# Optimization experiments

Hardware: AMD Instinct MI355X
Metric: run time of the kernel (lower is better)

The kernel has to match this reference:

```python
import jax, jax.numpy as jnp
import numpy as np

LAYERS = 2      # LightGCN propagation layers
LAMB = 0.5      # aux loss weight
REG = 1e-4      # embedding reg weight
N_AUX = 2       # len(behaviors) - 1


def setup_inputs() -> dict:
    key = jax.random.key(0)
    k = jax.random.split(key, 8)
    n_users, n_items, d = 100000, 50000, 32
    E = 1000000
    user_emb = (jax.random.normal(k[0], (n_users + 1, d), jnp.float32) * 0.1).at[0].set(0.0)
    item_emb = (jax.random.normal(k[1], (n_items + 1, d), jnp.float32) * 0.1).at[0].set(0.0)
    aux_u = jax.random.randint(k[2], (N_AUX, E), 1, n_users + 1)
    aux_i = jax.random.randint(k[3], (N_AUX, E), 1, n_items + 1)
    aux_edges = jnp.stack([aux_u, aux_i], axis=-1).astype(jnp.int32)
    tgt_u = jax.random.randint(k[4], (E,), 1, n_users + 1)
    tgt_i = jax.random.randint(k[5], (E,), 1, n_items + 1)
    target_edges = jnp.stack([tgt_u, tgt_i], axis=-1).astype(jnp.int32)
    # [B, 1+N_AUX, 3]: per row (user, pos_item, neg_item) for target then each aux behavior
    batch_data = jax.random.randint(k[6], (4096, 1 + N_AUX, 3), 1, n_items + 1).astype(jnp.int32)
    return {"user_emb": user_emb, "item_emb": item_emb, "batch_data": batch_data,
            "aux_edges": aux_edges, "target_edges": target_edges}


def _graph(edges, n_user_rows, N):
    """Symmetric-normalized bipartite LightGCN graph as directed COO (src, dst, w)."""
    u = edges[:, 0]
    v = edges[:, 1] + n_user_rows  # shift item ids into joint node space
    ones = jnp.ones(u.shape[0], jnp.float32)
    deg = jax.ops.segment_sum(ones, u, num_segments=N) + jax.ops.segment_sum(ones, v, num_segments=N)
    dinv = jnp.where(deg > 0, jax.lax.rsqrt(jnp.maximum(deg, 1.0)), 0.0)
    w = dinv[u] * dinv[v]
    src = jnp.concatenate([u, v])
    dst = jnp.concatenate([v, u])
    w2 = jnp.concatenate([w, w])
    return src, dst, w2


def _lightgcn(emb, src, dst, w, N):
    """L-layer LightGCN propagation, mean over layers 0..L."""
    acc = emb
    cur = emb
    for _ in range(LAYERS):
        cur = jax.ops.segment_sum(w[:, None] * cur[src], dst, num_segments=N)
        acc = acc + cur
    return acc / (LAYERS + 1)


def _prob(ue, ie, u, i):
    return jax.nn.relu(jnp.sum(ue[u] * ie[i], axis=-1))


def _bpr(p, n):
    return -jnp.mean(jax.nn.log_sigmoid(p - n))


def reference(user_emb, item_emb, batch_data, aux_edges, target_edges):
    Nu = user_emb.shape[0]
    N = Nu + item_emb.shape[0]
    all_emb = jnp.concatenate([user_emb, item_emb], axis=0)
    tgt_g = _graph(target_edges, Nu, N)

    user, p_item, n_item = batch_data[:, 0, 0], batch_data[:, 0, 1], batch_data[:, 0, 2]
    aux_user, aux_p, aux_n = batch_data[:, 1:, 0], batch_data[:, 1:, 1], batch_data[:, 1:, 2]

    cps, cns, dps, dns, aps, ans, aux_losses = [], [], [], [], [], [], []
    for idx in range(N_AUX):
        # combine graph = aux behavior edges union target edges
        comb_edges = jnp.concatenate([aux_edges[idx], target_edges], axis=0)
        ce = _lightgcn(all_emb, *_graph(comb_edges, Nu, N), N)
        cu, ci = ce[:Nu], ce[Nu:]
        cps.append(_prob(cu, ci, user, p_item))
        cns.append(_prob(cu, ci, user, n_item))

        ae = _lightgcn(all_emb, *_graph(aux_edges[idx], Nu, N), N)
        au, ai = ae[:Nu], ae[Nu:]
        aps.append(_prob(au, ai, user, p_item))
        ans.append(_prob(au, ai, user, n_item))

        # condition: propagate aux embeddings through the target graph
        de = _lightgcn(ae, *tgt_g, N)
        du, di = de[:Nu], de[Nu:]
        dps.append(_prob(du, di, user, p_item))
        dns.append(_prob(du, di, user, n_item))

        ps = jnp.sum(au[aux_user[:, idx]] * ai[aux_p[:, idx]], axis=-1)
        ns = jnp.sum(au[aux_user[:, idx]] * ai[aux_n[:, idx]], axis=-1)
        aux_losses.append(_bpr(ps, ns))

    aux_loss = jnp.mean(jnp.stack(aux_losses))

    def front_door(cond, comb, aux):
        return jnp.sum(cond * jnp.sum(comb * aux, axis=0), axis=0)

    p_scores = front_door(jnp.stack(dps), jnp.stack(cps), jnp.stack(aps))
    n_scores = front_door(jnp.stack(dns), jnp.stack(cns), jnp.stack(ans))
    rec_loss = _bpr(p_scores, n_scores)
    emb_loss = (jnp.linalg.norm(user_emb) + jnp.linalg.norm(item_emb)) / item_emb.shape[0]
    return rec_loss + LAMB * aux_loss + REG * emb_loss
```

## Files before the change

kernel.cpp:

```cpp
#include <hip/hip_runtime.h>
#include <hip/hip_fp16.h>
#include <math.h>

#define D 32
#define ROWU 16
#define NBK 1024
#define BSHIFT 8
#define TILE_H 16384
#define TILE_BIN 2048

typedef unsigned int u32;
typedef unsigned short u16;

__device__ __forceinline__ float logsigf(float x) {
  return fminf(x, 0.f) - log1pf(expf(-fabsf(x)));
}

__device__ __forceinline__ float lo16(u32 u) { return __uint_as_float(u << 16); }
__device__ __forceinline__ float hi16(u32 u) { return __uint_as_float(u & 0xFFFF0000u); }
__device__ __forceinline__ u32 pk2(float a, float b) {
  u32 ua = __float_as_uint(a), ub = __float_as_uint(b);
  u32 ra = (ua + 0x7FFFu + ((ua >> 16) & 1u)) >> 16;
  u32 rb = (ub + 0x7FFFu + ((ub >> 16) & 1u)) >> 16;
  return (ra & 0xFFFFu) | (rb << 16);
}
__device__ __forceinline__ float bfat(const u16* __restrict__ p, size_t off) {
  return __uint_as_float(((u32)p[off]) << 16);
}
__device__ __forceinline__ void accum8(float* a, float w, uint4 x) {
  a[0] += w * lo16(x.x); a[1] += w * hi16(x.x);
  a[2] += w * lo16(x.y); a[3] += w * hi16(x.y);
  a[4] += w * lo16(x.z); a[5] += w * hi16(x.z);
  a[6] += w * lo16(x.w); a[7] += w * hi16(x.w);
}
__device__ __forceinline__ uint4 pack8(const float* a, float w) {
  return make_uint4(pk2(w * a[0], w * a[1]), pk2(w * a[2], w * a[3]),
                    pk2(w * a[4], w * a[5]), pk2(w * a[6], w * a[7]));
}

__device__ __forceinline__ int wpack(float a, float b) {
  __half2 h = __floats2half2_rn(a, b);
  return *reinterpret_cast<int*>(&h);
}
__device__ __forceinline__ float2 hun(int wb) {
  __half2 h;
  *reinterpret_cast<int*>(&h) = wb;
  return __half22float2(h);
}


__global__ void hist_kernel(const int2* __restrict__ tgt, const int2* __restrict__ aux,
                            int E, int Nu, int BPS, int* __restrict__ bcur) {
  __shared__ int lh[NBK];
  int seg = blockIdx.x / BPS;
  int blk = blockIdx.x - seg * BPS;
  const int2* edges = (seg == 0) ? tgt : aux + (size_t)(seg - 1) * E;
  for (int b = threadIdx.x; b < NBK; b += 256) lh[b] = 0;
  __syncthreads();
  int e0 = blk * TILE_H;
  for (int k = threadIdx.x; k < TILE_H; k += 256) {
    int e = e0 + k;
    if (e < E) {
      int2 ed = edges[e];
      atomicAdd(&lh[ed.x >> BSHIFT], 1);
      atomicAdd(&lh[(ed.y + Nu) >> BSHIFT], 1);
    }
  }
  __syncthreads();
  for (int b = threadIdx.x; b < NBK; b += 256)
    if (lh[b]) atomicAdd(&bcur[seg * NBK + b], lh[b]);
}

__global__ void bscan_kernel(int* __restrict__ bcur) {
  int* b = bcur + blockIdx.x * NBK;
  int lane = threadIdx.x;
  int carry = 0;
  for (int base = 0; base < NBK; base += 64) {
    int i = base + lane;
    int v = b[i];
    int s = v;
    #pragma unroll
    for (int o = 1; o < 64; o <<= 1) {
      int t = __shfl_up(s, o);
      if (lane >= o) s += t;
    }
    b[i] = carry + s - v;
    carry += __shfl(s, 63);
  }
}

__global__ void bin_kernel(const int2* __restrict__ tgt, const int2* __restrict__ aux,
                           int E, int Nu, int BPS, int* __restrict__ bcur,
                           int* __restrict__ binned) {
  __shared__ int stage[2 * TILE_BIN];
  __shared__ int lh[NBK];
  __shared__ int loff[NBK];
  __shared__ int gb[NBK];
  __shared__ int wred[4];
  __shared__ int stot;
  int seg = blockIdx.x / BPS;
  int blk = blockIdx.x - seg * BPS;
  const int2* edges = (seg == 0) ? tgt : aux + (size_t)(seg - 1) * E;
  int* out = binned + (size_t)seg * 2 * E;
  int tid = threadIdx.x;
  for (int b = tid; b < NBK; b += 256) lh[b] = 0;
  __syncthreads();
  int e0 = blk * TILE_BIN;
  int pkv[16];
  int pb[16];
  int pr[16];
  #pragma unroll
  for (int it = 0; it < 8; ++it) {
    int e = e0 + tid + it * 256;
    bool ok = e < E;
    int2 ed = ok ? edges[e] : make_int2(0, -Nu);
    int u = ed.x, v = ed.y + Nu;
    int b1 = u >> BSHIFT, b2 = v >> BSHIFT;
    pkv[2 * it] = ((u & 255) << 18) | v;
    pb[2 * it] = b1;
    pr[2 * it] = ok ? atomicAdd(&lh[b1], 1) : 0;
    pkv[2 * it + 1] = ((v & 255) << 18) | u;
    pb[2 * it + 1] = b2;
    pr[2 * it + 1] = ok ? atomicAdd(&lh[b2], 1) : 0;
  }
  __syncthreads();
  int lane = tid & 63, wid = tid >> 6;
  int b4 = tid * 4;
  int v0 = lh[b4], v1 = lh[b4 + 1], v2 = lh[b4 + 2], v3 = lh[b4 + 3];
  int tsum = v0 + v1 + v2 + v3;
  int incl = tsum;
  #pragma unroll
  for (int o = 1; o < 64; o <<= 1) {
    int t = __shfl_up(incl, o);
    if (lane >= o) incl += t;
  }
  if (lane == 63) wred[wid] = incl;
  __syncthreads();
  int wbase = 0;
  for (int w = 0; w < wid; ++w) wbase += wred[w];
  int excl = wbase + incl - tsum;
  loff[b4] = excl;
  loff[b4 + 1] = excl + v0;
  loff[b4 + 2] = excl + v0 + v1;
  loff[b4 + 3] = excl + v0 + v1 + v2;
  if (tid == 255) stot = excl + tsum;
  #pragma unroll
  for (int j = 0; j < 4; ++j) {
    int b = b4 + j;
    int c = lh[b];
    gb[b] = c ? atomicAdd(&bcur[seg * NBK + b], c) : 0;
  }
  __syncthreads();
  #pragma unroll
  for (int it = 0; it < 16; ++it) {
    int e = e0 + tid + (it >> 1) * 256;
    if (e < E) stage[loff[pb[it]] + pr[it]] = pkv[it];
  }
  __syncthreads();
  int tot = stot;
  for (int k = tid; k < tot; k += 256) {
    int lo = 0, hi = NBK;
    while (lo < hi) {
      int mid = (lo + hi) >> 1;
      if (loff[mid] <= k) lo = mid + 1; else hi = mid;
    }
    int b = lo - 1;
    out[gb[b] + (k - loff[b])] = stage[k];
  }
}

__global__ void csr_count_kernel(const int* __restrict__ binned,
                                 const int* __restrict__ bend, int E2, int N, int NBKe,
                                 int* __restrict__ deg3, int* __restrict__ rp3) {
  __shared__ int cnt[256];
  __shared__ int wred[4];
  int seg = blockIdx.x / NBKe;
  int bkt = blockIdx.x - seg * NBKe;
  int node0 = bkt << BSHIFT;
  const int* bc = bend + seg * NBK;
  int start = (bkt == 0) ? 0 : bc[bkt - 1];
  int end = bc[bkt];
  int cntE = end - start;
  const int* src = binned + (size_t)seg * E2 + start;
  cnt[threadIdx.x] = 0;
  __syncthreads();
  for (int k = threadIdx.x; k < cntE; k += 256) atomicAdd(&cnt[src[k] >> 18], 1);
  __syncthreads();
  int lane = threadIdx.x & 63, wid = threadIdx.x >> 6;
  int v = cnt[threadIdx.x];
  int incl = v;
  #pragma unroll
  for (int o = 1; o < 64; o <<= 1) {
    int t = __shfl_up(incl, o);
    if (lane >= o) incl += t;
  }
  if (lane == 63) wred[wid] = incl;
  __syncthreads();
  int wbase = 0;
  for (int w = 0; w < wid; ++w) wbase += wred[w];
  int node = node0 + (int)threadIdx.x;
  if (node < N) {
    deg3[(size_t)seg * N + node] = v;
    rp3[(size_t)seg * (N + 1) + node] = start + wbase + incl - v;
  }
  if (bkt == 0 && threadIdx.x == 0) rp3[(size_t)seg * (N + 1) + N] = E2;
}

__global__ void dinv_all_kernel(const int* __restrict__ deg3, float* __restrict__ dinv5,
                                int N) {
  int n = blockIdx.x * blockDim.x + threadIdx.x;
  if (n >= N) return;
  int dt = deg3[n], d0 = deg3[N + n], d1 = deg3[2 * N + n];
  dinv5[n]         = dt ? rsqrtf((float)dt) : 0.f;
  dinv5[N + n]     = d0 ? rsqrtf((float)d0) : 0.f;
  dinv5[2 * N + n] = d1 ? rsqrtf((float)d1) : 0.f;
  int c0 = dt + d0, c1 = dt + d1;
  dinv5[3 * N + n] = c0 ? rsqrtf((float)c0) : 0.f;
  dinv5[4 * N + n] = c1 ? rsqrtf((float)c1) : 0.f;
}

__global__ void csr_scatter_kernel(const int* __restrict__ binned,
                                   const int* __restrict__ bend,
                                   const int* __restrict__ rp3,
                                   const float* __restrict__ dinv5,
                                   int E2, int N, int NBKe,
                                   int2* __restrict__ pk) {
  __shared__ int cnt[256];
  __shared__ int off[256];
  int seg = blockIdx.x / NBKe;
  int bkt = blockIdx.x - seg * NBKe;
  int node0 = bkt << BSHIFT;
  const int* bc = bend + seg * NBK;
  int start = (bkt == 0) ? 0 : bc[bkt - 1];
  int end = bc[bkt];
  int cntE = end - start;
  const int* src = binned + (size_t)seg * E2 + start;
  int node = node0 + (int)threadIdx.x;
  off[threadIdx.x] = (node < N) ? rp3[(size_t)seg * (N + 1) + node] : 0;
  cnt[threadIdx.x] = 0;
  const float* dvL = dinv5 + (size_t)(seg == 0 ? 3 : seg) * N;
  const float* dvH = dinv5 + (size_t)(seg == 0 ? 4 : seg + 2) * N;
  __syncthreads();
  int2* out = pk + (size_t)seg * E2;
  for (int k = threadIdx.x; k < cntE; k += 256) {
    int en = src[k];
    int lb = en >> 18;
    int c = en & 0x3FFFF;
    int pos = atomicAdd(&cnt[lb], 1);
    out[off[lb] + pos] = make_int2(c, wpack(dvL[c], dvH[c]));
  }
}

__global__ void cvt_emb_kernel(const float2* __restrict__ ue, long nu2,
                               const float2* __restrict__ ie, long ni2,
                               u32* __restrict__ emb) {
  long i = (long)blockIdx.x * blockDim.x + threadIdx.x;
  if (i >= nu2 + ni2) return;
  float2 v = (i < nu2) ? ue[i] : ie[i - nu2];
  emb[i] = pk2(v.x, v.y);
}


__global__ void gather_fused_all_kernel(const int* __restrict__ rp3,
                                        const int2* __restrict__ pk,
                                        const float* __restrict__ dinv5,
                                        const uint4* __restrict__ emb,
                                        uint4* __restrict__ BaAll, uint4* __restrict__ BcAll,
                                        int N, int E2) {
  const int* rpA0 = rp3 + (size_t)(N + 1);
  const int* rpA1 = rp3 + 2 * (size_t)(N + 1);
  const int2* pT = pk;
  const int2* pA0 = pk + (size_t)E2;
  const int2* pA1 = pk + 2 * (size_t)E2;
  const float* dvA0 = dinv5 + (size_t)N;
  const float* dvA1 = dinv5 + 2 * (size_t)N;
  const float* dvC0 = dinv5 + 3 * (size_t)N;
  const float* dvC1 = dinv5 + 4 * (size_t)N;
  int t = blockIdx.x * blockDim.x + threadIdx.x;
  int n = t >> 2;
  if (n >= N) return;
  int lane = t & 3;
  int qb = (threadIdx.x & 63) & 60;
  float aA0[8] = {0, 0, 0, 0, 0, 0, 0, 0};
  float aA1[8] = {0, 0, 0, 0, 0, 0, 0, 0};
  float aC0[8] = {0, 0, 0, 0, 0, 0, 0, 0};
  float aC1[8] = {0, 0, 0, 0, 0, 0, 0, 0};
  int s = rpA0[n], e = rpA0[n + 1];
  int j = s;
  for (; j + 3 < e; j += 4) {
    int2 en = pA0[j + lane];
    #pragma unroll
    for (int q = 0; q < 4; ++q) {
      int c = __shfl(en.x, qb + q);
      float2 w = hun(__shfl(en.y, qb + q));
      uint4 x = emb[(size_t)c * 4 + lane];
      accum8(aA0, w.x, x);
      accum8(aC0, w.y, x);
    }
  }
  for (; j < e; ++j) {
    int2 en = pA0[j];
    float2 w = hun(en.y);
    uint4 x = emb[(size_t)en.x * 4 + lane];
    accum8(aA0, w.x, x);
    accum8(aC0, w.y, x);
  }
  s = rpA1[n]; e = rpA1[n + 1];
  j = s;
  for (; j + 3 < e; j += 4) {
    int2 en = pA1[j + lane];
    #pragma unroll
    for (int q = 0; q < 4; ++q) {
      int c = __shfl(en.x, qb + q);
      float2 w = hun(__shfl(en.y, qb + q));
      uint4 x = emb[(size_t)c * 4 + lane];
      accum8(aA1, w.x, x);
      accum8(aC1, w.y, x);
    }
  }
  for (; j < e; ++j) {
    int2 en = pA1[j];
    float2 w = hun(en.y);
    uint4 x = emb[(size_t)en.x * 4 + lane];
    accum8(aA1, w.x, x);
    accum8(aC1, w.y, x);
  }
  s = rp3[n]; e = rp3[n + 1];
  j = s;
  for (; j + 3 < e; j += 4) {
    int2 en = pT[j + lane];
    #pragma unroll
    for (int q = 0; q < 4; ++q) {
      int c = __shfl(en.x, qb + q);
      float2 w = hun(__shfl(en.y, qb + q));
      uint4 x = emb[(size_t)c * 4 + lane];
      accum8(aC0, w.x, x);
      accum8(aC1, w.y, x);
    }
  }
  for (; j < e; ++j) {
    int2 en = pT[j];
    float2 w = hun(en.y);
    uint4 x = emb[(size_t)en.x * 4 + lane];
    accum8(aC0, w.x, x);
    accum8(aC1, w.y, x);
  }
  size_t o = (size_t)n * 4 + lane;
  size_t rowN4 = (size_t)N * 4;
  BaAll[o] = pack8(aA0, dvA0[n]);
  BaAll[rowN4 + o] = pack8(aA1, dvA1[n]);
  BcAll[o] = pack8(aC0, dvC0[n]);
  BcAll[rowN4 + o] = pack8(aC1, dvC1[n]);
}

__global__ void gather_avg_kernel(const int* __restrict__ rp3, const int2* __restrict__ pk,
                                  const float* __restrict__ dinv5,
                                  const uint4* __restrict__ emb,
                                  const uint4* __restrict__ BaAll, uint4* __restrict__ AI,
                                  int N, int E2) {
  int idx = blockIdx.y;
  const int* rp = rp3 + (size_t)(1 + idx) * (N + 1);
  const int2* pA = pk + (size_t)(1 + idx) * E2;
  const float* dv = dinv5 + (size_t)(1 + idx) * N;
  const uint4* cur = BaAll + (size_t)idx * N * 4;
  int t = blockIdx.x * blockDim.x + threadIdx.x;
  int n = t >> 2;
  if (n >= N) return;
  int lane = t & 3;
  int qb = (threadIdx.x & 63) & 60;
  float acc[8] = {0, 0, 0, 0, 0, 0, 0, 0};
  int s = rp[n], e = rp[n + 1];
  int j = s;
  for (; j + 3 < e; j += 4) {
    int2 en = pA[j + lane];
    #pragma unroll
    for (int q = 0; q < 4; ++q) {
      int c = __shfl(en.x, qb + q);
      float2 w = hun(__shfl(en.y, qb + q));
      uint4 x = cur[(size_t)c * 4 + lane];
      accum8(acc, w.x, x);
    }
  }
  for (; j < e; ++j) {
    int2 en = pA[j];
    float2 w = hun(en.y);
    uint4 x = cur[(size_t)en.x * 4 + lane];
    accum8(acc, w.x, x);
  }
  float wn = dv[n];
  uint4 e4 = emb[(size_t)n * 4 + lane];
  uint4 b4 = cur[(size_t)n * 4 + lane];
  float r[8];
  r[0] = (lo16(e4.x) + lo16(b4.x) + wn * acc[0]) * (1.f / 3.f);
  r[1] = (hi16(e4.x) + hi16(b4.x) + wn * acc[1]) * (1.f / 3.f);
  r[2] = (lo16(e4.y) + lo16(b4.y) + wn * acc[2]) * (1.f / 3.f);
  r[3] = (hi16(e4.y) + hi16(b4.y) + wn * acc[3]) * (1.f / 3.f);
  r[4] = (lo16(e4.z) + lo16(b4.z) + wn * acc[4]) * (1.f / 3.f);
  r[5] = (hi16(e4.z) + hi16(b4.z) + wn * acc[5]) * (1.f / 3.f);
  r[6] = (lo16(e4.w) + lo16(b4.w) + wn * acc[6]) * (1.f / 3.f);
  r[7] = (hi16(e4.w) + hi16(b4.w) + wn * acc[7]) * (1.f / 3.f);
  AI[(size_t)n * 8 + idx * 4 + lane] = pack8(r, 1.f);
}

__global__ void de_gather_kernel(const int* __restrict__ rp3, const int2* __restrict__ pk,
                                 const float* __restrict__ dinv5,
                                 const uint4* __restrict__ AI, uint4* __restrict__ DeI,
                                 int N) {
  int t = blockIdx.x * blockDim.x + threadIdx.x;
  int n = t >> 3;
  if (n >= N) return;
  int lane = t & 7;
  int gb = (threadIdx.x & 63) & 56;
  float acc[8] = {0, 0, 0, 0, 0, 0, 0, 0};
  int s = rp3[n], e = rp3[n + 1];
  int j = s;
  for (; j + 3 < e; j += 4) {
    int2 en = pk[j + (lane & 3)];
    #pragma unroll
    for (int q = 0; q < 4; ++q) {
      int c = __shfl(en.x, gb + q);
      float w = dinv5[c];
      uint4 x = AI[(size_t)c * 8 + lane];
      accum8(acc, w, x);
    }
  }
  for (; j < e; ++j) {
    int2 en = pk[j];
    float w = dinv5[en.x];
    uint4 x = AI[(size_t)en.x * 8 + lane];
    accum8(acc, w, x);
  }
  DeI[(size_t)n * 8 + lane] = pack8(acc, dinv5[n]);
}


__device__ __forceinline__ float fdim2(const int2* __restrict__ pkA, const int2* __restrict__ pkT,
                                       const int* __restrict__ rpA, const int* __restrict__ rpT,
                                       int idx, const float* __restrict__ dv,
                                       const u16* __restrict__ base, const u16* __restrict__ L1,
                                       int r, int d) {
  float acc = 0.f;
  for (int j = rpA[r]; j < rpA[r + 1]; ++j) {
    int2 en = pkA[j];
    acc += hun(en.y).y * bfat(L1, (size_t)en.x * D + d);
  }
  for (int j = rpT[r]; j < rpT[r + 1]; ++j) {
    int2 en = pkT[j];
    float2 w = hun(en.y);
    acc += (idx ? w.y : w.x) * bfat(L1, (size_t)en.x * D + d);
  }
  return (bfat(base, (size_t)r * D + d) + bfat(L1, (size_t)r * D + d) + dv[r] * acc) * (1.f / 3.f);
}

__device__ __forceinline__ float fdim1i(const int2* __restrict__ pkT, const int* __restrict__ rp,
                                        const float* __restrict__ dv,
                                        const u16* __restrict__ base, const u16* __restrict__ L1,
                                        int r, int di) {
  float acc = 0.f;
  for (int j = rp[r]; j < rp[r + 1]; ++j) {
    int2 en = pkT[j];
    acc += dv[en.x] * bfat(L1, (size_t)en.x * 64 + di);
  }
  return (bfat(base, (size_t)r * 64 + di) + bfat(L1, (size_t)r * 64 + di) + dv[r] * acc) * (1.f / 3.f);
}

__global__ void ce_sparse_kernel(const int* __restrict__ rp3, const int2* __restrict__ pk,
                                 const float* __restrict__ dinv5,
                                 const u32* __restrict__ EMBu, const u32* __restrict__ BcAll,
                                 const int* __restrict__ batch, int Bsz, int Nu, int N, int E2,
                                 float* __restrict__ cps, float* __restrict__ cns) {
  int idx = blockIdx.y;
  const int* rpA = rp3 + (size_t)(1 + idx) * (N + 1);
  const int2* pkA = pk + (size_t)(1 + idx) * E2;
  const float* dv = dinv5 + (size_t)(3 + idx) * N;
  const u16* base = (const u16*)EMBu;
  const u16* L1 = (const u16*)(BcAll + (size_t)idx * N * ROWU);
  float* outp = cps + (size_t)idx * Bsz;
  float* outn = cns + (size_t)idx * Bsz;
  int t = blockIdx.x * blockDim.x + threadIdx.x;
  int b = t >> 5, d = t & 31;
  if (b >= Bsz) return;
  int u = batch[b * 9 + 0];
  int p = batch[b * 9 + 1] + Nu;
  int n = batch[b * 9 + 2] + Nu;
  float uv = fdim2(pkA, pk, rpA, rp3, idx, dv, base, L1, u, d);
  float pv = fdim2(pkA, pk, rpA, rp3, idx, dv, base, L1, p, d);
  float nv = fdim2(pkA, pk, rpA, rp3, idx, dv, base, L1, n, d);
  float sp = uv * pv, sn = uv * nv;
  #pragma unroll
  for (int o = 16; o > 0; o >>= 1) {
    sp += __shfl_down(sp, o, 32);
    sn += __shfl_down(sn, o, 32);
  }
  if (d == 0) {
    outp[b] = fmaxf(sp, 0.f);
    outn[b] = fmaxf(sn, 0.f);
  }
}

__global__ void de_sparse_kernel(const int* __restrict__ rp3, const int2* __restrict__ pk,
                                 const float* __restrict__ dinv5,
                                 const u32* __restrict__ AI, const u32* __restrict__ DeI,
                                 const int* __restrict__ batch, int Bsz, int Nu, int N,
                                 float* __restrict__ dps, float* __restrict__ dns) {
  int idx = blockIdx.y;
  const u16* base = (const u16*)AI;
  const u16* L1 = (const u16*)DeI;
  float* outp = dps + (size_t)idx * Bsz;
  float* outn = dns + (size_t)idx * Bsz;
  int t = blockIdx.x * blockDim.x + threadIdx.x;
  int b = t >> 5, d = t & 31;
  if (b >= Bsz) return;
  int di = idx * 32 + d;
  int u = batch[b * 9 + 0];
  int p = batch[b * 9 + 1] + Nu;
  int n = batch[b * 9 + 2] + Nu;
  float uv = fdim1i(pk, rp3, dinv5, base, L1, u, di);
  float pv = fdim1i(pk, rp3, dinv5, base, L1, p, di);
  float nv = fdim1i(pk, rp3, dinv5, base, L1, n, di);
  float sp = uv * pv, sn = uv * nv;
  #pragma unroll
  for (int o = 16; o > 0; o >>= 1) {
    sp += __shfl_down(sp, o, 32);
    sn += __shfl_down(sn, o, 32);
  }
  if (d == 0) {
    outp[b] = fmaxf(sp, 0.f);
    outn[b] = fmaxf(sn, 0.f);
  }
}


__device__ __forceinline__ float dotrow(const u32* __restrict__ a, const u32* __restrict__ b) {
  float s = 0.f;
  #pragma unroll
  for (int k = 0; k < ROWU; ++k) {
    u32 x = a[k], y = b[k];
    s += lo16(x) * lo16(y) + hi16(x) * hi16(y);
  }
  return s;
}

__global__ void score_aux_kernel(const u32* __restrict__ AI, const int* __restrict__ batch,
                                 int Bsz, int Nu, int N, float* __restrict__ aps,
                                 float* __restrict__ ans_, float* __restrict__ accs) {
  int idx = blockIdx.y;
  const u32* A = AI + (size_t)idx * ROWU;
  float* outp = aps + (size_t)idx * Bsz;
  float* outn = ans_ + (size_t)idx * Bsz;
  int b = blockIdx.x * blockDim.x + threadIdx.x;
  float l = 0.f;
  if (b < Bsz) {
    int u = batch[b * 9 + 0];
    int p = batch[b * 9 + 1] + Nu;
    int n = batch[b * 9 + 2] + Nu;
    const u32* ur = A + (size_t)u * 32;
    outp[b] = fmaxf(dotrow(ur, A + (size_t)p * 32), 0.f);
    outn[b] = fmaxf(dotrow(ur, A + (size_t)n * 32), 0.f);
    const int* r = batch + b * 9 + 3 * (1 + idx);
    const u32* aur = A + (size_t)r[0] * 32;
    float ps = dotrow(aur, A + (size_t)(r[1] + Nu) * 32);
    float ns = dotrow(aur, A + (size_t)(r[2] + Nu) * 32);
    l = -logsigf(ps - ns);
  }
  for (int o = 32; o > 0; o >>= 1) l += __shfl_down(l, o);
  if ((threadIdx.x & 63) == 0) atomicAdd(&accs[idx], l);
}

__global__ void recloss_kernel(const float* __restrict__ cps, const float* __restrict__ cns,
                               const float* __restrict__ aps, const float* __restrict__ ans_,
                               const float* __restrict__ dps, const float* __restrict__ dns,
                               int Bsz, int NA, float* __restrict__ acc) {
  int b = blockIdx.x * blockDim.x + threadIdx.x;
  float l = 0.f;
  if (b < Bsz) {
    float dp = 0.f, dn = 0.f, cap = 0.f, can = 0.f;
    for (int i = 0; i < NA; ++i) {
      dp += dps[i * Bsz + b];
      dn += dns[i * Bsz + b];
      cap += cps[i * Bsz + b] * aps[i * Bsz + b];
      can += cns[i * Bsz + b] * ans_[i * Bsz + b];
    }
    l = -logsigf(dp * cap - dn * can);
  }
  for (int o = 32; o > 0; o >>= 1) l += __shfl_down(l, o);
  if ((threadIdx.x & 63) == 0) atomicAdd(acc, l);
}

__global__ void sumsq2_kernel(const float4* __restrict__ xu, int n4u,
                              const float4* __restrict__ xi, int n4i,
                              float* __restrict__ accU, float* __restrict__ accI) {
  __shared__ float redU[4], redI[4];
  int tid = threadIdx.x;
  int gid = blockIdx.x * blockDim.x + tid;
  int stride = gridDim.x * blockDim.x;
  float su = 0.f, si = 0.f;
  for (int i = gid; i < n4u; i += stride) {
    float4 v = xu[i];
    su += v.x * v.x + v.y * v.y + v.z * v.z + v.w * v.w;
  }
  for (int i = gid; i < n4i; i += stride) {
    float4 v = xi[i];
    si += v.x * v.x + v.y * v.y + v.z * v.z + v.w * v.w;
  }
  for (int o = 32; o > 0; o >>= 1) {
    su += __shfl_down(su, o);
    si += __shfl_down(si, o);
  }
  if ((tid & 63) == 0) { redU[tid >> 6] = su; redI[tid >> 6] = si; }
  __syncthreads();
  if (tid == 0) {
    atomicAdd(accU, redU[0] + redU[1] + redU[2] + redU[3]);
    atomicAdd(accI, redI[0] + redI[1] + redI[2] + redI[3]);
  }
}

__global__ void final_kernel(const float* __restrict__ accs, int Bsz, int NA, int NiRows,
                             float* __restrict__ out) {
  float rec = accs[NA] / (float)Bsz;
  float aux = 0.f;
  for (int i = 0; i < NA; ++i) aux += accs[i] / (float)Bsz;
  aux /= (float)NA;
  float embl = (sqrtf(accs[NA + 1]) + sqrtf(accs[NA + 2])) / (float)NiRows;
  out[0] = rec + 0.5f * aux + 1e-4f * embl;
}

extern "C" void kernel_launch(void* const* d_in, const int* in_sizes, int n_in,
                              void* d_out, int out_size, void* d_ws, size_t ws_size,
                              hipStream_t stream) {
  const float* user_emb = (const float*)d_in[0];
  const float* item_emb = (const float*)d_in[1];
  const int* batch = (const int*)d_in[2];
  const int* aux_edges = (const int*)d_in[3];
  const int* tgt_edges = (const int*)d_in[4];

  const int NuRows = in_sizes[0] / D;
  const int NiRows = in_sizes[1] / D;
  const int Bsz = in_sizes[2] / 9;
  const int E = in_sizes[4] / 2;
  const int NA = in_sizes[3] / (2 * E);
  const int N = NuRows + NiRows;
  const int E2 = 2 * E;
  const size_t rowH = (size_t)N * ROWU;
  const int BPS_H = (E + TILE_H - 1) / TILE_H;
  const int BPS_B = (E + TILE_BIN - 1) / TILE_BIN;
  const int NBKe = (N + (1 << BSHIFT) - 1) >> BSHIFT;

  u32* EMBu = (u32*)d_ws;
  u32* AI = EMBu + rowH;
  u32* BaAll = AI + 2 * rowH;
  u32* BcAll = BaAll + 2 * rowH;
  int* deg3 = (int*)(BcAll + 2 * rowH);
  float* dinv5 = (float*)(deg3 + 3 * (size_t)N);
  int* rp3 = (int*)(dinv5 + 5 * (size_t)N);
  int* bcur = rp3 + 3 * (size_t)(N + 1);
  uintptr_t pka = ((uintptr_t)(bcur + 3 * (size_t)NBK) + 7) & ~(uintptr_t)7;
  int2* pk = (int2*)pka;
  float* cps = (float*)(pk + 3 * (size_t)E2);
  float* cns = cps + (size_t)NA * Bsz;
  float* aps = cns + (size_t)NA * Bsz;
  float* ans_ = aps + (size_t)NA * Bsz;
  float* dps = ans_ + (size_t)NA * Bsz;
  float* dns = dps + (size_t)NA * Bsz;
  float* accs = dns + (size_t)NA * Bsz;
  int* binned = (int*)AI;

  const int TB = 256;
  const int gN = (N + TB - 1) / TB;
  const int gN4 = (N * 4 + TB - 1) / TB;
  const int gN8 = (N * 8 + TB - 1) / TB;
  const int gB = (Bsz + TB - 1) / TB;
  const int gB32 = (Bsz * 32 + TB - 1) / TB;
  const long nu2 = (long)NuRows * ROWU;
  const long ni2 = (long)NiRows * ROWU;
  const int gCvt = (int)((nu2 + ni2 + TB - 1) / TB);

  cvt_emb_kernel<<<gCvt, TB, 0, stream>>>((const float2*)user_emb, nu2,
                                          (const float2*)item_emb, ni2, EMBu);

  hipMemsetAsync(bcur, 0, 3 * (size_t)NBK * sizeof(int), stream);
  hist_kernel<<<3 * BPS_H, TB, 0, stream>>>((const int2*)tgt_edges, (const int2*)aux_edges,
                                            E, NuRows, BPS_H, bcur);
  bscan_kernel<<<3, 64, 0, stream>>>(bcur);
  bin_kernel<<<3 * BPS_B, TB, 0, stream>>>((const int2*)tgt_edges, (const int2*)aux_edges,
                                           E, NuRows, BPS_B, bcur, binned);
  csr_count_kernel<<<3 * NBKe, TB, 0, stream>>>(binned, bcur, E2, N, NBKe, deg3, rp3);
  dinv_all_kernel<<<gN, TB, 0, stream>>>(deg3, dinv5, N);
  csr_scatter_kernel<<<3 * NBKe, TB, 0, stream>>>(binned, bcur, rp3, dinv5, E2, N, NBKe, pk);

  hipMemsetAsync(accs, 0, (size_t)(NA + 3) * sizeof(float), stream);

  dim3 gridG(gN4, NA), gridB(gB, NA), gridS(gB32, NA);

  gather_fused_all_kernel<<<gN4, TB, 0, stream>>>(rp3, pk, dinv5, (const uint4*)EMBu,
                                                  (uint4*)BaAll, (uint4*)BcAll, N, E2);
  gather_avg_kernel<<<gridG, TB, 0, stream>>>(rp3, pk, dinv5, (const uint4*)EMBu,
                                              (const uint4*)BaAll, (uint4*)AI, N, E2);
  score_aux_kernel<<<gridB, TB, 0, stream>>>(AI, batch, Bsz, NuRows, N, aps, ans_, accs);
  ce_sparse_kernel<<<gridS, TB, 0, stream>>>(rp3, pk, dinv5, EMBu, BcAll,
                                             batch, Bsz, NuRows, N, E2, cps, cns);
  de_gather_kernel<<<gN8, TB, 0, stream>>>(rp3, pk, dinv5, (const uint4*)AI,
                                           (uint4*)BaAll, N);
  de_sparse_kernel<<<gridS, TB, 0, stream>>>(rp3, pk, dinv5, AI, (const u32*)BaAll,
                                             batch, Bsz, NuRows, N, dps, dns);

  sumsq2_kernel<<<104, TB, 0, stream>>>((const float4*)user_emb,
                                        (int)((size_t)NuRows * D / 4),
                                        (const float4*)item_emb,
                                        (int)((size_t)NiRows * D / 4),
                                        accs + NA + 1, accs + NA + 2);
  recloss_kernel<<<gB, TB, 0, stream>>>(cps, cns, aps, ans_, dps, dns, Bsz, NA, accs + NA);
  final_kernel<<<1, 1, 0, stream>>>(accs, Bsz, NA, NiRows, (float*)d_out);
}
```

Before: 668.0 us.

## Vectorize CSR edge loads, store bucket ids in bin stage, precompute weight table

```diff
diff --git a/kernel.cpp b/kernel.cpp
--- a/kernel.cpp
+++ b/kernel.cpp
@@ -38,9 +38,9 @@
                     pk2(w * a[4], w * a[5]), pk2(w * a[6], w * a[7]));
 }
 
-__device__ __forceinline__ int wpack(float a, float b) {
+__device__ __forceinline__ u32 wpack(float a, float b) {
   __half2 h = __floats2half2_rn(a, b);
-  return *reinterpret_cast<int*>(&h);
+  return *reinterpret_cast<u32*>(&h);
 }
 __device__ __forceinline__ float2 hun(int wb) {
   __half2 h;
@@ -93,6 +93,7 @@
                            int E, int Nu, int BPS, int* __restrict__ bcur,
                            int* __restrict__ binned) {
   __shared__ int stage[2 * TILE_BIN];
+  __shared__ u16 stagebk[2 * TILE_BIN];
   __shared__ int lh[NBK];
   __shared__ int loff[NBK];
   __shared__ int gb[NBK];
@@ -154,17 +155,16 @@
   #pragma unroll
   for (int it = 0; it < 16; ++it) {
     int e = e0 + tid + (it >> 1) * 256;
-    if (e < E) stage[loff[pb[it]] + pr[it]] = pkv[it];
+    if (e < E) {
+      int pos = loff[pb[it]] + pr[it];
+      stage[pos] = pkv[it];
+      stagebk[pos] = (u16)pb[it];
+    }
   }
   __syncthreads();
   int tot = stot;
   for (int k = tid; k < tot; k += 256) {
-    int lo = 0, hi = NBK;
-    while (lo < hi) {
-      int mid = (lo + hi) >> 1;
-      if (loff[mid] <= k) lo = mid + 1; else hi = mid;
-    }
-    int b = lo - 1;
+    int b = stagebk[k];
     out[gb[b] + (k - loff[b])] = stage[k];
   }
 }
@@ -207,22 +207,30 @@
 }
 
 __global__ void dinv_all_kernel(const int* __restrict__ deg3, float* __restrict__ dinv5,
-                                int N) {
+                                u32* __restrict__ wtab, int N) {
   int n = blockIdx.x * blockDim.x + threadIdx.x;
   if (n >= N) return;
   int dt = deg3[n], d0 = deg3[N + n], d1 = deg3[2 * N + n];
-  dinv5[n]         = dt ? rsqrtf((float)dt) : 0.f;
-  dinv5[N + n]     = d0 ? rsqrtf((float)d0) : 0.f;
-  dinv5[2 * N + n] = d1 ? rsqrtf((float)d1) : 0.f;
+  float wt  = dt ? rsqrtf((float)dt) : 0.f;
+  float wa0 = d0 ? rsqrtf((float)d0) : 0.f;
+  float wa1 = d1 ? rsqrtf((float)d1) : 0.f;
   int c0 = dt + d0, c1 = dt + d1;
-  dinv5[3 * N + n] = c0 ? rsqrtf((float)c0) : 0.f;
-  dinv5[4 * N + n] = c1 ? rsqrtf((float)c1) : 0.f;
+  float wc0 = c0 ? rsqrtf((float)c0) : 0.f;
+  float wc1 = c1 ? rsqrtf((float)c1) : 0.f;
+  dinv5[n] = wt;
+  dinv5[N + n] = wa0;
+  dinv5[2 * N + n] = wa1;
+  dinv5[3 * N + n] = wc0;
+  dinv5[4 * N + n] = wc1;
+  wtab[n] = wpack(wc0, wc1);
+  wtab[N + n] = wpack(wa0, wc0);
+  wtab[2 * N + n] = wpack(wa1, wc1);
 }
 
 __global__ void csr_scatter_kernel(const int* __restrict__ binned,
                                    const int* __restrict__ bend,
                                    const int* __restrict__ rp3,
-                                   const float* __restrict__ dinv5,
+                                   const u32* __restrict__ wtab,
                                    int E2, int N, int NBKe,
                                    int2* __restrict__ pk) {
   __shared__ int cnt[256];
@@ -238,8 +246,7 @@
   int node = node0 + (int)threadIdx.x;
   off[threadIdx.x] = (node < N) ? rp3[(size_t)seg * (N + 1) + node] : 0;
   cnt[threadIdx.x] = 0;
-  const float* dvL = dinv5 + (size_t)(seg == 0 ? 3 : seg) * N;
-  const float* dvH = dinv5 + (size_t)(seg == 0 ? 4 : seg + 2) * N;
+  const u32* wt = wtab + (size_t)seg * N;
   __syncthreads();
   int2* out = pk + (size_t)seg * E2;
   for (int k = threadIdx.x; k < cntE; k += 256) {
@@ -247,7 +254,7 @@
     int lb = en >> 18;
     int c = en & 0x3FFFF;
     int pos = atomicAdd(&cnt[lb], 1);
-    out[off[lb] + pos] = make_int2(c, wpack(dvL[c], dvH[c]));
+    out[off[lb] + pos] = make_int2(c, (int)wt[c]);
   }
 }
 
@@ -260,6 +267,38 @@
   emb[i] = pk2(v.x, v.y);
 }
 
+
+__device__ __forceinline__ void edge1_dual(const int2* __restrict__ p, int j, int lane,
+                                           const uint4* __restrict__ rows,
+                                           float* a1, float* a2) {
+  int2 en = p[j];
+  float2 w = hun(en.y);
+  uint4 x = rows[(size_t)en.x * 4 + lane];
+  accum8(a1, w.x, x);
+  accum8(a2, w.y, x);
+}
+
+__device__ __forceinline__ void stream_dual(const int* __restrict__ rp,
+                                            const int2* __restrict__ p, int n, int lane,
+                                            const uint4* __restrict__ rows,
+                                            float* a1, float* a2) {
+  int j = rp[n], e = rp[n + 1];
+  if ((j & 1) && j < e) { edge1_dual(p, j, lane, rows, a1, a2); ++j; }
+  for (; j + 3 < e; j += 4) {
+    int4 m0 = *reinterpret_cast<const int4*>(p + j);
+    int4 m1 = *reinterpret_cast<const int4*>(p + j + 2);
+    uint4 x0 = rows[(size_t)m0.x * 4 + lane];
+    uint4 x1 = rows[(size_t)m0.z * 4 + lane];
+    uint4 x2 = rows[(size_t)m1.x * 4 + lane];
+    uint4 x3 = rows[(size_t)m1.z * 4 + lane];
+    float2 w0 = hun(m0.y), w1 = hun(m0.w), w2 = hun(m1.y), w3 = hun(m1.w);
+    accum8(a1, w0.x, x0); accum8(a2, w0.y, x0);
+    accum8(a1, w1.x, x1); accum8(a2, w1.y, x1);
+    accum8(a1, w2.x, x2); accum8(a2, w2.y, x2);
+    accum8(a1, w3.x, x3); accum8(a2, w3.y, x3);
+  }
+  for (; j < e; ++j) edge1_dual(p, j, lane, rows, a1, a2);
+}
 
 __global__ void gather_fused_all_kernel(const int* __restrict__ rp3,
                                         const int2* __restrict__ pk,
@@ -280,71 +319,13 @@
   int n = t >> 2;
   if (n >= N) return;
   int lane = t & 3;
-  int qb = (threadIdx.x & 63) & 60;
   float aA0[8] = {0, 0, 0, 0, 0, 0, 0, 0};
   float aA1[8] = {0, 0, 0, 0, 0, 0, 0, 0};
   float aC0[8] = {0, 0, 0, 0, 0, 0, 0, 0};
   float aC1[8] = {0, 0, 0, 0, 0, 0, 0, 0};
-  int s = rpA0[n], e = rpA0[n + 1];
-  int j = s;
-  for (; j + 3 < e; j += 4) {
-    int2 en = pA0[j + lane];
-    #pragma unroll
-    for (int q = 0; q < 4; ++q) {
-      int c = __shfl(en.x, qb + q);
-      float2 w = hun(__shfl(en.y, qb + q));
-      uint4 x = emb[(size_t)c * 4 + lane];
-      accum8(aA0, w.x, x);
-      accum8(aC0, w.y, x);
-    }
-  }
-  for (; j < e; ++j) {
-    int2 en = pA0[j];
-    float2 w = hun(en.y);
-    uint4 x = emb[(size_t)en.x * 4 + lane];
-    accum8(aA0, w.x, x);
-    accum8(aC0, w.y, x);
-  }
-  s = rpA1[n]; e = rpA1[n + 1];
-  j = s;
-  for (; j + 3 < e; j += 4) {
-    int2 en = pA1[j + lane];
-    #pragma unroll
-    for (int q = 0; q < 4; ++q) {
-      int c = __shfl(en.x, qb + q);
-      float2 w = hun(__shfl(en.y, qb + q));
-      uint4 x = emb[(size_t)c * 4 + lane];
-      accum8(aA1, w.x, x);
-      accum8(aC1, w.y, x);
-    }
-  }
-  for (; j < e; ++j) {
-    int2 en = pA1[j];
-    float2 w = hun(en.y);
-    uint4 x = emb[(size_t)en.x * 4 + lane];
-    accum8(aA1, w.x, x);
-    accum8(aC1, w.y, x);
-  }
-  s = rp3[n]; e = rp3[n + 1];
-  j = s;
-  for (; j + 3 < e; j += 4) {
-    int2 en = pT[j + lane];
-    #pragma unroll
-    for (int q = 0; q < 4; ++q) {
-      int c = __shfl(en.x, qb + q);
-      float2 w = hun(__shfl(en.y, qb + q));
-      uint4 x = emb[(size_t)c * 4 + lane];
-      accum8(aC0, w.x, x);
-      accum8(aC1, w.y, x);
-    }
-  }
-  for (; j < e; ++j) {
-    int2 en = pT[j];
-    float2 w = hun(en.y);
-    uint4 x = emb[(size_t)en.x * 4 + lane];
-    accum8(aC0, w.x, x);
-    accum8(aC1, w.y, x);
-  }
+  stream_dual(rpA0, pA0, n, lane, emb, aA0, aC0);
+  stream_dual(rpA1, pA1, n, lane, emb, aA1, aC1);
+  stream_dual(rp3, pT, n, lane, emb, aC0, aC1);
   size_t o = (size_t)n * 4 + lane;
   size_t rowN4 = (size_t)N * 4;
   BaAll[o] = pack8(aA0, dvA0[n]);
@@ -367,25 +348,30 @@
   int n = t >> 2;
   if (n >= N) return;
   int lane = t & 3;
-  int qb = (threadIdx.x & 63) & 60;
   float acc[8] = {0, 0, 0, 0, 0, 0, 0, 0};
-  int s = rp[n], e = rp[n + 1];
-  int j = s;
+  int j = rp[n], e = rp[n + 1];
+  if ((j & 1) && j < e) {
+    int2 en = pA[j];
+    uint4 x = cur[(size_t)en.x * 4 + lane];
+    accum8(acc, hun(en.y).x, x);
+    ++j;
+  }
   for (; j + 3 < e; j += 4) {
-    int2 en = pA[j + lane];
-    #pragma unroll
-    for (int q = 0; q < 4; ++q) {
-      int c = __shfl(en.x, qb + q);
-      float2 w = hun(__shfl(en.y, qb + q));
-      uint4 x = cur[(size_t)c * 4 + lane];
-      accum8(acc, w.x, x);
-    }
+    int4 m0 = *reinterpret_cast<const int4*>(pA + j);
+    int4 m1 = *reinterpret_cast<const int4*>(pA + j + 2);
+    uint4 x0 = cur[(size_t)m0.x * 4 + lane];
+    uint4 x1 = cur[(size_t)m0.z * 4 + lane];
+    uint4 x2 = cur[(size_t)m1.x * 4 + lane];
+    uint4 x3 = cur[(size_t)m1.z * 4 + lane];
+    accum8(acc, hun(m0.y).x, x0);
+    accum8(acc, hun(m0.w).x, x1);
+    accum8(acc, hun(m1.y).x, x2);
+    accum8(acc, hun(m1.w).x, x3);
   }
   for (; j < e; ++j) {
     int2 en = pA[j];
-    float2 w = hun(en.y);
     uint4 x = cur[(size_t)en.x * 4 + lane];
-    accum8(acc, w.x, x);
+    accum8(acc, hun(en.y).x, x);
   }
   float wn = dv[n];
   uint4 e4 = emb[(size_t)n * 4 + lane];
@@ -410,25 +396,30 @@
   int n = t >> 3;
   if (n >= N) return;
   int lane = t & 7;
-  int gb = (threadIdx.x & 63) & 56;
   float acc[8] = {0, 0, 0, 0, 0, 0, 0, 0};
-  int s = rp3[n], e = rp3[n + 1];
-  int j = s;
+  int j = rp3[n], e = rp3[n + 1];
+  if ((j & 1) && j < e) {
+    int c = pk[j].x;
+    uint4 x = AI[(size_t)c * 8 + lane];
+    accum8(acc, dinv5[c], x);
+    ++j;
+  }
   for (; j + 3 < e; j += 4) {
-    int2 en = pk[j + (lane & 3)];
-    #pragma unroll
-    for (int q = 0; q < 4; ++q) {
-      int c = __shfl(en.x, gb + q);
-      float w = dinv5[c];
-      uint4 x = AI[(size_t)c * 8 + lane];
-      accum8(acc, w, x);
-    }
+    int4 m0 = *reinterpret_cast<const int4*>(pk + j);
+    int4 m1 = *reinterpret_cast<const int4*>(pk + j + 2);
+    uint4 x0 = AI[(size_t)m0.x * 8 + lane];
+    uint4 x1 = AI[(size_t)m0.z * 8 + lane];
+    uint4 x2 = AI[(size_t)m1.x * 8 + lane];
+    uint4 x3 = AI[(size_t)m1.z * 8 + lane];
+    accum8(acc, dinv5[m0.x], x0);
+    accum8(acc, dinv5[m0.z], x1);
+    accum8(acc, dinv5[m1.x], x2);
+    accum8(acc, dinv5[m1.z], x3);
   }
   for (; j < e; ++j) {
-    int2 en = pk[j];
-    float w = dinv5[en.x];
-    uint4 x = AI[(size_t)en.x * 8 + lane];
-    accum8(acc, w, x);
+    int c = pk[j].x;
+    uint4 x = AI[(size_t)c * 8 + lane];
+    accum8(acc, dinv5[c], x);
   }
   DeI[(size_t)n * 8 + lane] = pack8(acc, dinv5[n]);
 }
@@ -652,9 +643,10 @@
   u32* BcAll = BaAll + 2 * rowH;
   int* deg3 = (int*)(BcAll + 2 * rowH);
   float* dinv5 = (float*)(deg3 + 3 * (size_t)N);
-  int* rp3 = (int*)(dinv5 + 5 * (size_t)N);
+  u32* wtab = (u32*)(dinv5 + 5 * (size_t)N);
+  int* rp3 = (int*)(wtab + 3 * (size_t)N);
   int* bcur = rp3 + 3 * (size_t)(N + 1);
-  uintptr_t pka = ((uintptr_t)(bcur + 3 * (size_t)NBK) + 7) & ~(uintptr_t)7;
+  uintptr_t pka = ((uintptr_t)(bcur + 3 * (size_t)NBK) + 15) & ~(uintptr_t)15;
   int2* pk = (int2*)pka;
   float* cps = (float*)(pk + 3 * (size_t)E2);
   float* cns = cps + (size_t)NA * Bsz;
@@ -685,8 +677,8 @@
   bin_kernel<<<3 * BPS_B, TB, 0, stream>>>((const int2*)tgt_edges, (const int2*)aux_edges,
                                            E, NuRows, BPS_B, bcur, binned);
   csr_count_kernel<<<3 * NBKe, TB, 0, stream>>>(binned, bcur, E2, N, NBKe, deg3, rp3);
-  dinv_all_kernel<<<gN, TB, 0, stream>>>(deg3, dinv5, N);
-  csr_scatter_kernel<<<3 * NBKe, TB, 0, stream>>>(binned, bcur, rp3, dinv5, E2, N, NBKe, pk);
+  dinv_all_kernel<<<gN, TB, 0, stream>>>(deg3, dinv5, wtab, N);
+  csr_scatter_kernel<<<3 * NBKe, TB, 0, stream>>>(binned, bcur, rp3, wtab, E2, N, NBKe, pk);
 
   hipMemsetAsync(accs, 0, (size_t)(NA + 3) * sizeof(float), stream);
 
```

New measurement: 641.6 us. 1.04x faster.
